# Performance work log

Measured on AMD Instinct MI355X. Metric: run time of the kernel, lower is better.

The kernel has to match this reference:

```python
import jax, jax.numpy as jnp
import numpy as np

B, L, D = 4, 512, 512
VOCAB = 32000
SEMB_NUM = 4
SEG = VOCAB // SEMB_NUM
TEMP = float(np.power(512, 0.5))  # sqrt(d_model)
NEG_INF = 1e9  # hparams.inf
INIT_RANGE = 0.1


def setup_inputs() -> dict:
    key = jax.random.key(0)
    k1, k2, k3 = jax.random.split(key, 3)
    q = jax.random.normal(k1, (B, L, D), dtype=jnp.float32)
    x_rank = jax.random.randint(k2, (B, L), 0, SEMB_NUM)
    emb = jax.random.uniform(k3, (VOCAB, D), dtype=jnp.float32,
                             minval=-INIT_RANGE, maxval=INIT_RANGE)
    return {"q": q, "x_rank": x_rank, "emb": emb}


def reference(q, x_rank, emb):
    # segment id of each vocab entry: [V]
    seg_id = jnp.arange(VOCAB) // SEG
    # mask == True means "blocked": token with x_rank==i only sees segment i
    mask = seg_id[None, None, :] != x_rank[:, :, None]          # [B, L, V]
    scores = jnp.einsum('bld,vd->blv', q, emb) / TEMP           # [B, L, V]
    scores = jnp.where(mask, -NEG_INF, scores)
    attn = jax.nn.softmax(scores, axis=-1)
    attn = jnp.where(mask, 0.0, attn)  # masked_fill_ after softmax (dropout=0, eval)
    ctx = jnp.einsum('blv,vd->bld', attn, emb)                  # [B, L, D]
    return ctx + q  # residual add (no char_gate)
```

## Files before the change

kernel.cpp:

```cpp
#include <hip/hip_runtime.h>
#include <math.h>


constexpr int Dm   = 512;
constexpr int SEG  = 8000;
constexpr int PSTR = 8064;
constexpr int NTOK = 2048;
constexpr int TIL  = 128;
constexpr int MAXTILES = 20;
constexpr int MAXSLOTS = MAXTILES * TIL;

constexpr size_t WS_META  = 8192;
constexpr size_t WS_PERM  = 8448;
constexpr size_t WS_IPERM = 20480;
constexpr size_t WS_QB8   = 32768;
constexpr size_t WS_EB8   = WS_QB8 + (size_t)MAXSLOTS * Dm;
constexpr size_t WS_OACC  = WS_EB8 + (size_t)32000 * Dm;
constexpr size_t WS_ET8   = WS_OACC + (size_t)8 * Dm * MAXSLOTS * 2;
constexpr size_t WS_P8    = WS_ET8 + (size_t)Dm * 32000;
constexpr size_t WS_DPART = WS_P8 + (size_t)MAXSLOTS * PSTR;

typedef __attribute__((ext_vector_type(4))) float f32x4;
typedef __attribute__((ext_vector_type(4))) unsigned int u32x4;
#define LDSP __attribute__((address_space(3)))
typedef LDSP unsigned char lds_u8;
typedef LDSP u32x4 lds_v4;
typedef LDSP int lds_i32;

static __device__ __forceinline__ ushort f2bf(float f) {
    union { float f; unsigned u; } v; v.f = f;
    unsigned r = v.u + 0x7FFF + ((v.u >> 16) & 1);
    return (ushort)(r >> 16);
}
static __device__ __forceinline__ float bf2f(ushort u) {
    union { unsigned u; float f; } v; v.u = ((unsigned)u) << 16;
    return v.f;
}
static __device__ __forceinline__ int pack_fp8x4(float a, float b, float c, float d) {
    int r = __builtin_amdgcn_cvt_pk_fp8_f32(a, b, 0, false);
    r = __builtin_amdgcn_cvt_pk_fp8_f32(c, d, r, true);
    return r;
}

#define WAIT0 asm volatile("s_waitcnt vmcnt(0)" ::: "memory")
#define LGKM0 asm volatile("s_waitcnt lgkmcnt(0)" ::: "memory")
#define BARX  { __builtin_amdgcn_s_barrier(); __builtin_amdgcn_sched_barrier(0); }

#define CSTEP(CA, CB)                                                          \
    _Pragma("unroll")                                                          \
    for (int ks = 0; ks < 4; ++ks) {                                           \
        const int cg = ks*2 + (quad >> 1), ho = (quad & 1) * 8;                \
        long A[4], B[4];                                                       \
        _Pragma("unroll")                                                      \
        for (int m = 0; m < 4; ++m) {                                          \
            const int row = rh*64 + m*16 + l15;                                \
            A[m] = *(const LDSP long*)((CA) + (row*8 + (cg ^ (row & 7)))*16 + ho); \
        }                                                                      \
        _Pragma("unroll")                                                      \
        for (int n = 0; n < 4; ++n) {                                          \
            const int row = th*64 + n*16 + l15;                                \
            B[n] = *(const LDSP long*)((CB) + (row*8 + (cg ^ (row & 7)))*16 + ho); \
        }                                                                      \
        __builtin_amdgcn_s_setprio(1);                                         \
        _Pragma("unroll")                                                      \
        for (int m = 0; m < 4; ++m)                                            \
            _Pragma("unroll")                                                  \
            for (int n = 0; n < 4; ++n)                                        \
                acc[m][n] = __builtin_amdgcn_mfma_f32_16x16x32_fp8_fp8(A[m], B[n], acc[m][n], 0, 0, 0); \
        __builtin_amdgcn_s_setprio(0);                                         \
    }

#define PSTEP(CA, CB, NA, NB, T)                                               \
    {                                                                          \
        u32x4 sv[8];                                                           \
        _Pragma("unroll")                                                      \
        for (int i = 0; i < 4; ++i) {                                          \
            sv[i]   = *(const u32x4*)(srcA[i] + (size_t)(T)*128);              \
            sv[4+i] = *(const u32x4*)(srcB[i] + (size_t)(T)*128);              \
        }                                                                      \
        CSTEP(CA, CB)                                                          \
        WAIT0;                                                                 \
        _Pragma("unroll")                                                      \
        for (int i = 0; i < 4; ++i) {                                          \
            *(lds_v4*)((NA) + dst[i]) = sv[i];                                 \
            *(lds_v4*)((NB) + dst[i]) = sv[4+i];                               \
        }                                                                      \
        LGKM0; BARX;                                                           \
    }

#define PROLOG(DA, DB)                                                         \
    {                                                                          \
        u32x4 sv[8];                                                           \
        _Pragma("unroll")                                                      \
        for (int i = 0; i < 4; ++i) {                                          \
            sv[i]   = *(const u32x4*)(srcA[i]);                                \
            sv[4+i] = *(const u32x4*)(srcB[i]);                                \
        }                                                                      \
        WAIT0;                                                                 \
        _Pragma("unroll")                                                      \
        for (int i = 0; i < 4; ++i) {                                          \
            *(lds_v4*)((DA) + dst[i]) = sv[i];                                 \
            *(lds_v4*)((DB) + dst[i]) = sv[4+i];                               \
        }                                                                      \
        LGKM0; BARX;                                                           \
    }

__global__ __launch_bounds__(256)
void k_conv(const float* __restrict__ emb, unsigned char* __restrict__ EB8,
            unsigned char* __restrict__ ET8,
            const int* __restrict__ xr, int* __restrict__ meta,
            int* __restrict__ perm, int* __restrict__ iperm) {
    __shared__ unsigned char sT[64 * 8 * 16];
    const int tid = threadIdx.x;
    if (blockIdx.x == 250) {
        if (blockIdx.y != 0) return;
        __shared__ int cnt[4], base[5], cur[4];
        if (tid < 4) { cnt[tid] = 0; cur[tid] = 0; }
        __syncthreads();
        for (int t = tid; t < NTOK; t += 256)
            atomicAdd(&cnt[xr[t]], 1);
        __syncthreads();
        if (tid == 0) {
            base[0] = 0;
            for (int r = 0; r < 4; ++r) base[r+1] = base[r] + ((cnt[r] + TIL - 1) / TIL) * TIL;
            for (int r = 0; r < 5; ++r) meta[r] = base[r];
        }
        __syncthreads();
        for (int s = tid; s < MAXSLOTS; s += 256) perm[s] = -1;
        __syncthreads();
        for (int t = tid; t < NTOK; t += 256) {
            int r = xr[t];
            int sl = base[r] + atomicAdd(&cur[r], 1);
            perm[sl] = t;
            iperm[t] = sl;
        }
        return;
    }
    const int r0 = blockIdx.x * 128, d0 = blockIdx.y * 64;
    {
        const int dq = tid & 15, ro = tid >> 4;
        int p[8];
        #pragma unroll
        for (int i = 0; i < 8; ++i) {
            float4 v = *(const float4*)(emb + (size_t)(r0 + ro*8 + i) * Dm + d0 + dq*4);
            p[i] = pack_fp8x4(v.x, v.y, v.z, v.w);
            *(int*)(EB8 + (size_t)(r0 + ro*8 + i) * Dm + d0 + dq*4) = p[i];
        }
        const int gr = ro >> 1, half = ro & 1;
        #pragma unroll
        for (int j = 0; j < 4; ++j) {
            const int d = dq*4 + j;
            unsigned long long t = 0;
            #pragma unroll
            for (int i = 0; i < 8; ++i)
                t |= ((unsigned long long)((p[i] >> (8*j)) & 0xff)) << (8*i);
            *(unsigned long long*)(sT + (d*8 + (gr ^ (d & 7))) * 16 + half * 8) = t;
        }
    }
    __syncthreads();
    {
        const int d = tid >> 2, rq = tid & 3;
        unsigned char* dst = ET8 + (size_t)(d0 + d) * 32000 + r0;
        #pragma unroll
        for (int b = 0; b < 2; ++b) {
            const int gr = rq * 2 + b;
            *(uint4*)(dst + gr * 16) = *(const uint4*)(sT + (d*8 + (gr ^ (d & 7))) * 16);
        }
    }
}

__global__ __launch_bounds__(256)
void k_qb(const float* __restrict__ q, const int* __restrict__ perm,
          unsigned char* __restrict__ Qb8) {
    const int slot = blockIdx.x * 8 + (threadIdx.x >> 5);
    const int ln = threadIdx.x & 31;
    const int tok = perm[slot];
    #pragma unroll
    for (int j = 0; j < 4; ++j) {
        const int c4 = ln + j * 32;
        int p = 0;
        if (tok >= 0) {
            float4 v = ((const float4*)q)[(size_t)tok * 128 + c4];
            p = pack_fp8x4(v.x, v.y, v.z, v.w);
        }
        ((int*)(Qb8 + (size_t)slot * Dm))[c4] = p;
    }
}

__global__ __launch_bounds__(256, 2)
void k_qk(const unsigned char* __restrict__ EB8, const unsigned char* __restrict__ Qb8,
          const int* __restrict__ meta, float* __restrict__ dpart,
          unsigned char* __restrict__ P8) {
    __shared__ unsigned char sA0[128 * 128];
    __shared__ unsigned char sB0[128 * 128];
    __shared__ unsigned char sA1[128 * 128];
    __shared__ unsigned char sB1[128 * 128];
    const int tid = threadIdx.x, lane = tid & 63, w = tid >> 6;
    const int g    = blockIdx.x & 7;
    const int rest = blockIdx.x >> 3;
    const int tt       = rest >> 3;
    const int rt_local = rest & 7;
    const int c = g * 8 + rt_local;
    const int slot0 = tt * TIL;
    const int b1 = meta[1], b2 = meta[2], b3 = meta[3], b4 = meta[4];
    if (slot0 >= b4) return;
    const int row0 = c * 128;
    if (row0 >= PSTR) return;
    const int rank = (slot0 >= b1) + (slot0 >= b2) + (slot0 >= b3);

    const unsigned char* srcA[4];
    const unsigned char* srcB[4];
    int dst[4];
    #pragma unroll
    for (int i = 0; i < 4; ++i) {
        const int gg = w * 256 + i * 64 + lane;
        const int r = gg >> 3, cg = gg & 7;
        int grow = row0 + r;
        if (grow >= SEG) grow = SEG - 1;
        srcA[i] = EB8 + (size_t)rank * SEG * Dm + (size_t)grow * Dm + cg * 16;
        srcB[i] = Qb8 + (size_t)(slot0 + r) * Dm + cg * 16;
        dst[i]  = (r * 8 + (cg ^ (r & 7))) * 16;
    }
    const int rh = w >> 1, th = w & 1, quad = lane >> 4, l15 = lane & 15;
    const float invT = 0.04419417382415922f;
    lds_u8* a0 = (lds_u8*)sA0; lds_u8* b0 = (lds_u8*)sB0;
    lds_u8* a1 = (lds_u8*)sA1; lds_u8* b1p = (lds_u8*)sB1;

    f32x4 acc[4][4] = {};
    PROLOG(a0, b0)
    PSTEP(a0, b0, a1, b1p, 1)
    PSTEP(a1, b1p, a0, b0, 2)
    PSTEP(a0, b0, a1, b1p, 3)
    CSTEP(a1, b1p)

    lds_i32* pT = (lds_i32*)sA0;
    float dsum[4] = {0.f, 0.f, 0.f, 0.f};
    #pragma unroll
    for (int m = 0; m < 4; ++m) {
        const int rloc = rh*64 + m*16 + quad*4;
        const int r4 = row0 + rloc;
        const int r4i = rloc >> 2;
        #pragma unroll
        for (int n = 0; n < 4; ++n) {
            const int slot_l = th*64 + n*16 + l15;
            int pv = 0;
            if (r4 < SEG) {
                float e0 = __expf(acc[m][n][0] * invT);
                float e1 = __expf(acc[m][n][1] * invT);
                float e2 = __expf(acc[m][n][2] * invT);
                float e3 = __expf(acc[m][n][3] * invT);
                pv = pack_fp8x4(e0, e1, e2, e3);
                dsum[n] += e0 + e1 + e2 + e3;
            }
            pT[slot_l * 32 + (r4i ^ ((slot_l & 7) << 2))] = pv;
        }
    }
    BARX;
    #pragma unroll
    for (int p = 0; p < 4; ++p) {
        const int sr = (tid >> 3) + p * 32;
        const int c4 = (tid & 7) * 4;
        const int i0 = sr * 32 + (c4 ^ ((sr & 7) << 2));
        u32x4 v = *(const LDSP u32x4*)(pT + i0);
        *(u32x4*)(P8 + (size_t)(slot0 + sr) * PSTR + row0 + (tid & 7) * 16) = v;
    }
    #pragma unroll
    for (int n = 0; n < 4; ++n) {
        float s = dsum[n];
        s += __shfl_xor(s, 16, 64);
        s += __shfl_xor(s, 32, 64);
        if (quad == 0)
            dpart[(size_t)(c * 2 + rh) * MAXSLOTS + slot0 + th*64 + n*16 + l15] = s;
    }
}

__global__ __launch_bounds__(256, 2)
void k_pv(const unsigned char* __restrict__ ET8, const unsigned char* __restrict__ P8,
          const int* __restrict__ meta, ushort* __restrict__ Oacc) {
    __shared__ unsigned char sA0[128 * 128];
    __shared__ unsigned char sB0[128 * 128];
    __shared__ unsigned char sA1[128 * 128];
    __shared__ unsigned char sB1[128 * 128];
    const int tid = threadIdx.x, lane = tid & 63, w = tid >> 6;
    const int z    = blockIdx.x & 7;
    const int rest = blockIdx.x >> 3;
    const int tt   = rest >> 2;
    const int dt   = rest & 3;
    const int slot0 = tt * TIL;
    const int b1 = meta[1], b2 = meta[2], b3 = meta[3], b4 = meta[4];
    if (slot0 >= b4) return;
    const int rank = (slot0 >= b1) + (slot0 >= b2) + (slot0 >= b3);
    const int d0 = dt * 128;
    const int kstart = z * 1024;
    const int nit = (z == 7) ? 7 : 8;

    const unsigned char* srcA[4];
    const unsigned char* srcB[4];
    int dst[4];
    #pragma unroll
    for (int i = 0; i < 4; ++i) {
        const int gg = w * 256 + i * 64 + lane;
        const int r = gg >> 3, cg = gg & 7;
        srcA[i] = ET8 + (size_t)(d0 + r) * 32000 + (size_t)rank * SEG + kstart + cg * 16;
        srcB[i] = P8 + (size_t)(slot0 + r) * PSTR + kstart + cg * 16;
        dst[i]  = (r * 8 + (cg ^ (r & 7))) * 16;
    }
    const int rh = w >> 1, th = w & 1, quad = lane >> 4, l15 = lane & 15;
    lds_u8* cA = (lds_u8*)sA0; lds_u8* cB = (lds_u8*)sB0;
    lds_u8* nA = (lds_u8*)sA1; lds_u8* nB = (lds_u8*)sB1;

    f32x4 acc[4][4] = {};
    PROLOG(cA, cB)
    for (int t = 1; t < nit; ++t) {
        PSTEP(cA, cB, nA, nB, t)
        lds_u8* tp;
        tp = cA; cA = nA; nA = tp;
        tp = cB; cB = nB; nB = tp;
    }
    CSTEP(cA, cB)

    ushort* Oz = Oacc + (size_t)z * MAXSLOTS * Dm;
    #pragma unroll
    for (int m = 0; m < 4; ++m) {
        const int d4 = d0 + rh*64 + m*16 + quad*4;
        #pragma unroll
        for (int n = 0; n < 4; ++n) {
            const int slot = slot0 + th*64 + n*16 + l15;
            unsigned long long u =
                  (unsigned long long)f2bf(acc[m][n][0])
                | ((unsigned long long)f2bf(acc[m][n][1]) << 16)
                | ((unsigned long long)f2bf(acc[m][n][2]) << 32)
                | ((unsigned long long)f2bf(acc[m][n][3]) << 48);
            *(unsigned long long*)(Oz + (size_t)slot * Dm + d4) = u;
        }
    }
}

__global__ __launch_bounds__(256)
void k_final(const float* __restrict__ q, const int* __restrict__ iperm,
             const float* __restrict__ dpart, const ushort* __restrict__ Oacc,
             float* __restrict__ out) {
    const int tk = threadIdx.x >> 5;
    const int dl = threadIdx.x & 31;
    const int token = blockIdx.x * 8 + tk;
    const int s = iperm[token];
    float ds = 0.f;
    #pragma unroll
    for (int r = 0; r < 4; ++r) {
        const int j = dl + r * 32;
        if (j < 126) ds += dpart[(size_t)j * MAXSLOTS + s];
    }
    ds += __shfl_xor(ds, 1, 64);
    ds += __shfl_xor(ds, 2, 64);
    ds += __shfl_xor(ds, 4, 64);
    ds += __shfl_xor(ds, 8, 64);
    ds += __shfl_xor(ds, 16, 64);
    const float inv = 1.0f / ds;
    const float* qrow = q + (size_t)token * Dm;
    float* orow = out + (size_t)token * Dm;
    #pragma unroll
    for (int p = 0; p < 4; ++p) {
        const int d = p * 128 + dl * 4;
        float a0 = 0.f, a1 = 0.f, a2 = 0.f, a3 = 0.f;
        #pragma unroll
        for (int z = 0; z < 8; ++z) {
            unsigned long long u = *(const unsigned long long*)
                (Oacc + ((size_t)z * MAXSLOTS + s) * Dm + d);
            a0 += bf2f((ushort)u);
            a1 += bf2f((ushort)(u >> 16));
            a2 += bf2f((ushort)(u >> 32));
            a3 += bf2f((ushort)(u >> 48));
        }
        float4 qv = *(const float4*)(qrow + d);
        float4 o;
        o.x = a0 * inv + qv.x; o.y = a1 * inv + qv.y;
        o.z = a2 * inv + qv.z; o.w = a3 * inv + qv.w;
        *(float4*)(orow + d) = o;
    }
}

extern "C" void kernel_launch(void* const* d_in, const int* in_sizes, int n_in,
                              void* d_out, int out_size, void* d_ws, size_t ws_size,
                              hipStream_t stream) {
    const float* q   = (const float*)d_in[0];
    const int*   xr  = (const int*)d_in[1];
    const float* emb = (const float*)d_in[2];
    float* out = (float*)d_out;
    char* ws = (char*)d_ws;

    int*    meta         = (int*)(ws + WS_META);
    int*    perm         = (int*)(ws + WS_PERM);
    int*    iperm        = (int*)(ws + WS_IPERM);
    unsigned char* Qb8   = (unsigned char*)(ws + WS_QB8);
    unsigned char* EB8   = (unsigned char*)(ws + WS_EB8);
    ushort* Oacc         = (ushort*)(ws + WS_OACC);
    unsigned char* ET8   = (unsigned char*)(ws + WS_ET8);
    unsigned char* P8    = (unsigned char*)(ws + WS_P8);
    float*  dpart        = (float*)(ws + WS_DPART);

    k_conv<<<dim3(251, 8), 256, 0, stream>>>(emb, EB8, ET8, xr, meta, perm, iperm);
    k_qb<<<MAXSLOTS / 8, 256, 0, stream>>>(q, perm, Qb8);
    k_qk<<<8 * 8 * MAXTILES, 256, 0, stream>>>(EB8, Qb8, meta, dpart, P8);
    k_pv<<<8 * 4 * MAXTILES, 256, 0, stream>>>(ET8, P8, meta, Oacc);
    k_final<<<NTOK / 8, 256, 0, stream>>>(q, iperm, dpart, Oacc, out);
}
```

Baseline: 166.6 us.

## Enlarge QK and PV GEMM tiles to 256 rows with 64-wide K steps

Both fp8 MFMA kernels move from 128x128 tiles with 128-byte K steps to 256x128 tiles with 64-byte K steps. Each warp now holds an 8x4 accumulator grid, and the LDS swizzle and staging layout are changed to match. The grid sizes are halved and the dpart partial count in the final reduction shrinks to match. The aim is more operand reuse per LDS load and fewer blocks. The cost is more accumulator registers, which may reduce occupancy, and fewer blocks to spread across the CUs.

```diff
diff --git a/kernel.cpp b/kernel.cpp
--- a/kernel.cpp
+++ b/kernel.cpp
@@ -46,62 +46,64 @@
 #define LGKM0 asm volatile("s_waitcnt lgkmcnt(0)" ::: "memory")
 #define BARX  { __builtin_amdgcn_s_barrier(); __builtin_amdgcn_sched_barrier(0); }
 
-#define CSTEP(CA, CB)                                                          \
+#define CSTEP8(CA, CB)                                                         \
     _Pragma("unroll")                                                          \
-    for (int ks = 0; ks < 4; ++ks) {                                           \
+    for (int ks = 0; ks < 2; ++ks) {                                           \
         const int cg = ks*2 + (quad >> 1), ho = (quad & 1) * 8;                \
-        long A[4], B[4];                                                       \
+        long A[8], B[4];                                                       \
         _Pragma("unroll")                                                      \
-        for (int m = 0; m < 4; ++m) {                                          \
-            const int row = rh*64 + m*16 + l15;                                \
-            A[m] = *(const LDSP long*)((CA) + (row*8 + (cg ^ (row & 7)))*16 + ho); \
+        for (int m = 0; m < 8; ++m) {                                          \
+            const int row = rh*128 + m*16 + l15;                               \
+            A[m] = *(const LDSP long*)((CA) + (row*4 + (cg ^ (row & 3)))*16 + ho); \
         }                                                                      \
         _Pragma("unroll")                                                      \
         for (int n = 0; n < 4; ++n) {                                          \
             const int row = th*64 + n*16 + l15;                                \
-            B[n] = *(const LDSP long*)((CB) + (row*8 + (cg ^ (row & 7)))*16 + ho); \
+            B[n] = *(const LDSP long*)((CB) + (row*4 + (cg ^ (row & 3)))*16 + ho); \
         }                                                                      \
         __builtin_amdgcn_s_setprio(1);                                         \
         _Pragma("unroll")                                                      \
-        for (int m = 0; m < 4; ++m)                                            \
+        for (int m = 0; m < 8; ++m)                                            \
             _Pragma("unroll")                                                  \
             for (int n = 0; n < 4; ++n)                                        \
                 acc[m][n] = __builtin_amdgcn_mfma_f32_16x16x32_fp8_fp8(A[m], B[n], acc[m][n], 0, 0, 0); \
         __builtin_amdgcn_s_setprio(0);                                         \
     }
 
-#define PSTEP(CA, CB, NA, NB, T)                                               \
+#define PSTEP8(CA, CB, NA, NB, T)                                              \
     {                                                                          \
-        u32x4 sv[8];                                                           \
-        _Pragma("unroll")                                                      \
-        for (int i = 0; i < 4; ++i) {                                          \
-            sv[i]   = *(const u32x4*)(srcA[i] + (size_t)(T)*128);              \
-            sv[4+i] = *(const u32x4*)(srcB[i] + (size_t)(T)*128);              \
-        }                                                                      \
-        CSTEP(CA, CB)                                                          \
+        u32x4 sa0 = *(const u32x4*)(srcA[0] + (size_t)(T)*64);                 \
+        u32x4 sa1 = *(const u32x4*)(srcA[1] + (size_t)(T)*64);                 \
+        u32x4 sa2 = *(const u32x4*)(srcA[2] + (size_t)(T)*64);                 \
+        u32x4 sa3 = *(const u32x4*)(srcA[3] + (size_t)(T)*64);                 \
+        u32x4 sb0 = *(const u32x4*)(srcB[0] + (size_t)(T)*64);                 \
+        u32x4 sb1 = *(const u32x4*)(srcB[1] + (size_t)(T)*64);                 \
+        CSTEP8(CA, CB)                                                         \
         WAIT0;                                                                 \
-        _Pragma("unroll")                                                      \
-        for (int i = 0; i < 4; ++i) {                                          \
-            *(lds_v4*)((NA) + dst[i]) = sv[i];                                 \
-            *(lds_v4*)((NB) + dst[i]) = sv[4+i];                               \
-        }                                                                      \
+        *(lds_v4*)((NA) + dstA[0]) = sa0;                                      \
+        *(lds_v4*)((NA) + dstA[1]) = sa1;                                      \
+        *(lds_v4*)((NA) + dstA[2]) = sa2;                                      \
+        *(lds_v4*)((NA) + dstA[3]) = sa3;                                      \
+        *(lds_v4*)((NB) + dstB[0]) = sb0;                                      \
+        *(lds_v4*)((NB) + dstB[1]) = sb1;                                      \
         LGKM0; BARX;                                                           \
     }
 
-#define PROLOG(DA, DB)                                                         \
+#define PROLOG8(DA, DB)                                                        \
     {                                                                          \
-        u32x4 sv[8];                                                           \
-        _Pragma("unroll")                                                      \
-        for (int i = 0; i < 4; ++i) {                                          \
-            sv[i]   = *(const u32x4*)(srcA[i]);                                \
-            sv[4+i] = *(const u32x4*)(srcB[i]);                                \
-        }                                                                      \
+        u32x4 sa0 = *(const u32x4*)(srcA[0]);                                  \
+        u32x4 sa1 = *(const u32x4*)(srcA[1]);                                  \
+        u32x4 sa2 = *(const u32x4*)(srcA[2]);                                  \
+        u32x4 sa3 = *(const u32x4*)(srcA[3]);                                  \
+        u32x4 sb0 = *(const u32x4*)(srcB[0]);                                  \
+        u32x4 sb1 = *(const u32x4*)(srcB[1]);                                  \
         WAIT0;                                                                 \
-        _Pragma("unroll")                                                      \
-        for (int i = 0; i < 4; ++i) {                                          \
-            *(lds_v4*)((DA) + dst[i]) = sv[i];                                 \
-            *(lds_v4*)((DB) + dst[i]) = sv[4+i];                               \
-        }                                                                      \
+        *(lds_v4*)((DA) + dstA[0]) = sa0;                                      \
+        *(lds_v4*)((DA) + dstA[1]) = sa1;                                      \
+        *(lds_v4*)((DA) + dstA[2]) = sa2;                                      \
+        *(lds_v4*)((DA) + dstA[3]) = sa3;                                      \
+        *(lds_v4*)((DB) + dstB[0]) = sb0;                                      \
+        *(lds_v4*)((DB) + dstB[1]) = sb1;                                      \
         LGKM0; BARX;                                                           \
     }
 
@@ -191,55 +193,63 @@
 void k_qk(const unsigned char* __restrict__ EB8, const unsigned char* __restrict__ Qb8,
           const int* __restrict__ meta, float* __restrict__ dpart,
           unsigned char* __restrict__ P8) {
-    __shared__ unsigned char sA0[128 * 128];
-    __shared__ unsigned char sB0[128 * 128];
-    __shared__ unsigned char sA1[128 * 128];
-    __shared__ unsigned char sB1[128 * 128];
+    __shared__ unsigned char smem[49152];
+    lds_u8* A0 = (lds_u8*)smem;
+    lds_u8* A1 = (lds_u8*)(smem + 16384);
+    lds_u8* B0 = (lds_u8*)(smem + 32768);
+    lds_u8* B1 = (lds_u8*)(smem + 40960);
     const int tid = threadIdx.x, lane = tid & 63, w = tid >> 6;
     const int g    = blockIdx.x & 7;
     const int rest = blockIdx.x >> 3;
-    const int tt       = rest >> 3;
-    const int rt_local = rest & 7;
-    const int c = g * 8 + rt_local;
+    const int tt   = rest >> 2;
+    const int rt   = rest & 3;
+    const int c = g * 4 + rt;
     const int slot0 = tt * TIL;
     const int b1 = meta[1], b2 = meta[2], b3 = meta[3], b4 = meta[4];
     if (slot0 >= b4) return;
-    const int row0 = c * 128;
-    if (row0 >= PSTR) return;
+    const int row0 = c * 256;
     const int rank = (slot0 >= b1) + (slot0 >= b2) + (slot0 >= b3);
 
-    const unsigned char* srcA[4];
-    const unsigned char* srcB[4];
-    int dst[4];
+    const unsigned char* srcA[4]; int dstA[4];
     #pragma unroll
     for (int i = 0; i < 4; ++i) {
-        const int gg = w * 256 + i * 64 + lane;
-        const int r = gg >> 3, cg = gg & 7;
+        const int gg = i * 256 + tid;
+        const int r = gg >> 2, cg = gg & 3;
         int grow = row0 + r;
         if (grow >= SEG) grow = SEG - 1;
         srcA[i] = EB8 + (size_t)rank * SEG * Dm + (size_t)grow * Dm + cg * 16;
+        dstA[i] = (r * 4 + (cg ^ (r & 3))) * 16;
+    }
+    const unsigned char* srcB[2]; int dstB[2];
+    #pragma unroll
+    for (int i = 0; i < 2; ++i) {
+        const int gg = i * 256 + tid;
+        const int r = gg >> 2, cg = gg & 3;
         srcB[i] = Qb8 + (size_t)(slot0 + r) * Dm + cg * 16;
-        dst[i]  = (r * 8 + (cg ^ (r & 7))) * 16;
+        dstB[i] = (r * 4 + (cg ^ (r & 3))) * 16;
     }
     const int rh = w >> 1, th = w & 1, quad = lane >> 4, l15 = lane & 15;
     const float invT = 0.04419417382415922f;
-    lds_u8* a0 = (lds_u8*)sA0; lds_u8* b0 = (lds_u8*)sB0;
-    lds_u8* a1 = (lds_u8*)sA1; lds_u8* b1p = (lds_u8*)sB1;
-
-    f32x4 acc[4][4] = {};
-    PROLOG(a0, b0)
-    PSTEP(a0, b0, a1, b1p, 1)
-    PSTEP(a1, b1p, a0, b0, 2)
-    PSTEP(a0, b0, a1, b1p, 3)
-    CSTEP(a1, b1p)
-
-    lds_i32* pT = (lds_i32*)sA0;
+
+    f32x4 acc[8][4] = {};
+    PROLOG8(A0, B0)
+    PSTEP8(A0, B0, A1, B1, 1)
+    PSTEP8(A1, B1, A0, B0, 2)
+    PSTEP8(A0, B0, A1, B1, 3)
+    PSTEP8(A1, B1, A0, B0, 4)
+    PSTEP8(A0, B0, A1, B1, 5)
+    PSTEP8(A1, B1, A0, B0, 6)
+    PSTEP8(A0, B0, A1, B1, 7)
+    CSTEP8(A1, B1)
+    BARX
+
+    lds_i32* pT = (lds_i32*)smem;
     float dsum[4] = {0.f, 0.f, 0.f, 0.f};
     #pragma unroll
-    for (int m = 0; m < 4; ++m) {
-        const int rloc = rh*64 + m*16 + quad*4;
+    for (int m = 0; m < 8; ++m) {
+        const int rloc = rh*128 + m*16 + quad*4;
         const int r4 = row0 + rloc;
-        const int r4i = rloc >> 2;
+        const int gi = (rloc >> 4);
         #pragma unroll
         for (int n = 0; n < 4; ++n) {
             const int slot_l = th*64 + n*16 + l15;
@@ -252,17 +262,19 @@
                 pv = pack_fp8x4(e0, e1, e2, e3);
                 dsum[n] += e0 + e1 + e2 + e3;
             }
-            pT[slot_l * 32 + (r4i ^ ((slot_l & 7) << 2))] = pv;
+            pT[slot_l * 64 + ((gi ^ (slot_l & 15)) << 2) + quad] = pv;
         }
     }
     BARX;
     #pragma unroll
-    for (int p = 0; p < 4; ++p) {
-        const int sr = (tid >> 3) + p * 32;
-        const int c4 = (tid & 7) * 4;
-        const int i0 = sr * 32 + (c4 ^ ((sr & 7) << 2));
-        u32x4 v = *(const LDSP u32x4*)(pT + i0);
-        *(u32x4*)(P8 + (size_t)(slot0 + sr) * PSTR + row0 + (tid & 7) * 16) = v;
+    for (int p = 0; p < 8; ++p) {
+        const int sr = (tid >> 4) + p * 16;
+        const int gi = tid & 15;
+        const int col = row0 + gi * 16;
+        if (col < PSTR) {
+            u32x4 v = *(const LDSP u32x4*)(pT + sr * 64 + ((gi ^ (sr & 15)) << 2));
+            *(u32x4*)(P8 + (size_t)(slot0 + sr) * PSTR + col) = v;
+        }
     }
     #pragma unroll
     for (int n = 0; n < 4; ++n) {
@@ -277,52 +289,56 @@
 __global__ __launch_bounds__(256, 2)
 void k_pv(const unsigned char* __restrict__ ET8, const unsigned char* __restrict__ P8,
           const int* __restrict__ meta, ushort* __restrict__ Oacc) {
-    __shared__ unsigned char sA0[128 * 128];
-    __shared__ unsigned char sB0[128 * 128];
-    __shared__ unsigned char sA1[128 * 128];
-    __shared__ unsigned char sB1[128 * 128];
+    __shared__ unsigned char smem[49152];
     const int tid = threadIdx.x, lane = tid & 63, w = tid >> 6;
     const int z    = blockIdx.x & 7;
     const int rest = blockIdx.x >> 3;
-    const int tt   = rest >> 2;
-    const int dt   = rest & 3;
+    const int tt   = rest >> 1;
+    const int dt   = rest & 1;
     const int slot0 = tt * TIL;
     const int b1 = meta[1], b2 = meta[2], b3 = meta[3], b4 = meta[4];
     if (slot0 >= b4) return;
     const int rank = (slot0 >= b1) + (slot0 >= b2) + (slot0 >= b3);
-    const int d0 = dt * 128;
+    const int d0 = dt * 256;
     const int kstart = z * 1024;
-    const int nit = (z == 7) ? 7 : 8;
-
-    const unsigned char* srcA[4];
-    const unsigned char* srcB[4];
-    int dst[4];
+    const int nit = (z == 7) ? 14 : 16;
+
+    const unsigned char* srcA[4]; int dstA[4];
     #pragma unroll
     for (int i = 0; i < 4; ++i) {
-        const int gg = w * 256 + i * 64 + lane;
-        const int r = gg >> 3, cg = gg & 7;
+        const int gg = i * 256 + tid;
+        const int r = gg >> 2, cg = gg & 3;
         srcA[i] = ET8 + (size_t)(d0 + r) * 32000 + (size_t)rank * SEG + kstart + cg * 16;
+        dstA[i] = (r * 4 + (cg ^ (r & 3))) * 16;
+    }
+    const unsigned char* srcB[2]; int dstB[2];
+    #pragma unroll
+    for (int i = 0; i < 2; ++i) {
+        const int gg = i * 256 + tid;
+        const int r = gg >> 2, cg = gg & 3;
         srcB[i] = P8 + (size_t)(slot0 + r) * PSTR + kstart + cg * 16;
-        dst[i]  = (r * 8 + (cg ^ (r & 7))) * 16;
+        dstB[i] = (r * 4 + (cg ^ (r & 3))) * 16;
     }
     const int rh = w >> 1, th = w & 1, quad = lane >> 4, l15 = lane & 15;
-    lds_u8* cA = (lds_u8*)sA0; lds_u8* cB = (lds_u8*)sB0;
-    lds_u8* nA = (lds_u8*)sA1; lds_u8* nB = (lds_u8*)sB1;
-
-    f32x4 acc[4][4] = {};
-    PROLOG(cA, cB)
+    lds_u8* cA = (lds_u8*)smem;
+    lds_u8* nA = (lds_u8*)(smem + 16384);
+    lds_u8* cB = (lds_u8*)(smem + 32768);
+    lds_u8* nB = (lds_u8*)(smem + 40960);
+
+    f32x4 acc[8][4] = {};
+    PROLOG8(cA, cB)
     for (int t = 1; t < nit; ++t) {
-        PSTEP(cA, cB, nA, nB, t)
+        PSTEP8(cA, cB, nA, nB, t)
         lds_u8* tp;
         tp = cA; cA = nA; nA = tp;
         tp = cB; cB = nB; nB = tp;
     }
-    CSTEP(cA, cB)
+    CSTEP8(cA, cB)
 
     ushort* Oz = Oacc + (size_t)z * MAXSLOTS * Dm;
     #pragma unroll
-    for (int m = 0; m < 4; ++m) {
-        const int d4 = d0 + rh*64 + m*16 + quad*4;
+    for (int m = 0; m < 8; ++m) {
+        const int d4 = d0 + rh*128 + m*16 + quad*4;
         #pragma unroll
         for (int n = 0; n < 4; ++n) {
             const int slot = slot0 + th*64 + n*16 + l15;
@@ -346,9 +362,9 @@
     const int s = iperm[token];
     float ds = 0.f;
     #pragma unroll
-    for (int r = 0; r < 4; ++r) {
+    for (int r = 0; r < 2; ++r) {
         const int j = dl + r * 32;
-        if (j < 126) ds += dpart[(size_t)j * MAXSLOTS + s];
+        ds += dpart[(size_t)j * MAXSLOTS + s];
     }
     ds += __shfl_xor(ds, 1, 64);
     ds += __shfl_xor(ds, 2, 64);
@@ -400,7 +416,7 @@
 
     k_conv<<<dim3(251, 8), 256, 0, stream>>>(emb, EB8, ET8, xr, meta, perm, iperm);
     k_qb<<<MAXSLOTS / 8, 256, 0, stream>>>(q, perm, Qb8);
-    k_qk<<<8 * 8 * MAXTILES, 256, 0, stream>>>(EB8, Qb8, meta, dpart, P8);
-    k_pv<<<8 * 4 * MAXTILES, 256, 0, stream>>>(ET8, P8, meta, Oacc);
+    k_qk<<<8 * 4 * MAXTILES, 256, 0, stream>>>(EB8, Qb8, meta, dpart, P8);
+    k_pv<<<8 * 2 * MAXTILES, 256, 0, stream>>>(ET8, P8, meta, Oacc);
     k_final<<<NTOK / 8, 256, 0, stream>>>(q, iperm, dpart, Oacc, out);
 }
```

Result: slower. 182.1 us (+9.3%).

## Pre-tile fp8 operands into MFMA fragment layout and load directly to registers

Applied to the files above, without the earlier changes.

The producer kernels (k_conv, k_qb, k_qk's P output) now write the fp8 embedding, transposed embedding, query and probability matrices in a blocked layout that matches the MFMA operand fragment order. The GEMM kernels k_qk and k_pv drop their LDS double buffering and load 16-byte fragments straight from global memory into registers, using a triple-buffered register pipeline with no barriers. This removes LDS staging, bank-conflict swizzles and block syncs in the hot loops. In exchange the loads depend on global latency and cache hits, register pressure rises, and the producers need an extra LDS transpose pass.

```diff
diff --git a/kernel.cpp b/kernel.cpp
--- a/kernel.cpp
+++ b/kernel.cpp
@@ -4,7 +4,6 @@
 
 constexpr int Dm   = 512;
 constexpr int SEG  = 8000;
-constexpr int PSTR = 8064;
 constexpr int NTOK = 2048;
 constexpr int TIL  = 128;
 constexpr int MAXTILES = 20;
@@ -14,17 +13,16 @@
 constexpr size_t WS_PERM  = 8448;
 constexpr size_t WS_IPERM = 20480;
 constexpr size_t WS_QB8   = 32768;
-constexpr size_t WS_EB8   = WS_QB8 + (size_t)MAXSLOTS * Dm;
-constexpr size_t WS_OACC  = WS_EB8 + (size_t)32000 * Dm;
-constexpr size_t WS_ET8   = WS_OACC + (size_t)8 * Dm * MAXSLOTS * 2;
-constexpr size_t WS_P8    = WS_ET8 + (size_t)Dm * 32000;
-constexpr size_t WS_DPART = WS_P8 + (size_t)MAXSLOTS * PSTR;
+constexpr size_t WS_EB8   = WS_QB8 + (size_t)160 * 8 * 1024;
+constexpr size_t WS_OACC  = WS_EB8 + (size_t)2000 * 8 * 1024;
+constexpr size_t WS_ET8   = WS_OACC + (size_t)8 * MAXSLOTS * Dm * 2;
+constexpr size_t WS_P8    = WS_ET8 + (size_t)32 * 504 * 1024;
+constexpr size_t WS_DPART = WS_P8 + (size_t)160 * 128 * 1024;
 
 typedef __attribute__((ext_vector_type(4))) float f32x4;
-typedef __attribute__((ext_vector_type(4))) unsigned int u32x4;
+typedef __attribute__((ext_vector_type(2))) long l64x2;
 #define LDSP __attribute__((address_space(3)))
 typedef LDSP unsigned char lds_u8;
-typedef LDSP u32x4 lds_v4;
 typedef LDSP int lds_i32;
 
 static __device__ __forceinline__ ushort f2bf(float f) {
@@ -42,75 +40,39 @@
     return r;
 }
 
-#define WAIT0 asm volatile("s_waitcnt vmcnt(0)" ::: "memory")
-#define LGKM0 asm volatile("s_waitcnt lgkmcnt(0)" ::: "memory")
-#define BARX  { __builtin_amdgcn_s_barrier(); __builtin_amdgcn_sched_barrier(0); }
-
-#define CSTEP(CA, CB)                                                          \
-    _Pragma("unroll")                                                          \
-    for (int ks = 0; ks < 4; ++ks) {                                           \
-        const int cg = ks*2 + (quad >> 1), ho = (quad & 1) * 8;                \
-        long A[4], B[4];                                                       \
+#define LOADT(BUF, T)                                                          \
+    { _Pragma("unroll")                                                        \
+      for (int i = 0; i < 4; ++i) {                                            \
+        BUF##a[i] = *(const l64x2*)(pA[i] + ((size_t)(T) << 10));              \
+        BUF##b[i] = *(const l64x2*)(pB[i] + ((size_t)(T) << 10));              \
+      }                                                                        \
+      __builtin_amdgcn_sched_barrier(0); }
+
+#define CONLY(BUF)                                                             \
+    { __builtin_amdgcn_s_setprio(1);                                           \
+      _Pragma("unroll")                                                        \
+      for (int m = 0; m < 4; ++m)                                              \
         _Pragma("unroll")                                                      \
-        for (int m = 0; m < 4; ++m) {                                          \
-            const int row = rh*64 + m*16 + l15;                                \
-            A[m] = *(const LDSP long*)((CA) + (row*8 + (cg ^ (row & 7)))*16 + ho); \
-        }                                                                      \
+        for (int n = 0; n < 4; ++n)                                            \
+            acc[m][n] = __builtin_amdgcn_mfma_f32_16x16x32_fp8_fp8(            \
+                BUF##a[m][0], BUF##b[n][0], acc[m][n], 0, 0, 0);               \
+      _Pragma("unroll")                                                        \
+      for (int m = 0; m < 4; ++m)                                              \
         _Pragma("unroll")                                                      \
-        for (int n = 0; n < 4; ++n) {                                          \
-            const int row = th*64 + n*16 + l15;                                \
-            B[n] = *(const LDSP long*)((CB) + (row*8 + (cg ^ (row & 7)))*16 + ho); \
-        }                                                                      \
-        __builtin_amdgcn_s_setprio(1);                                         \
-        _Pragma("unroll")                                                      \
-        for (int m = 0; m < 4; ++m)                                            \
-            _Pragma("unroll")                                                  \
-            for (int n = 0; n < 4; ++n)                                        \
-                acc[m][n] = __builtin_amdgcn_mfma_f32_16x16x32_fp8_fp8(A[m], B[n], acc[m][n], 0, 0, 0); \
-        __builtin_amdgcn_s_setprio(0);                                         \
-    }
-
-#define PSTEP(CA, CB, NA, NB, T)                                               \
-    {                                                                          \
-        u32x4 sv[8];                                                           \
-        _Pragma("unroll")                                                      \
-        for (int i = 0; i < 4; ++i) {                                          \
-            sv[i]   = *(const u32x4*)(srcA[i] + (size_t)(T)*128);              \
-            sv[4+i] = *(const u32x4*)(srcB[i] + (size_t)(T)*128);              \
-        }                                                                      \
-        CSTEP(CA, CB)                                                          \
-        WAIT0;                                                                 \
-        _Pragma("unroll")                                                      \
-        for (int i = 0; i < 4; ++i) {                                          \
-            *(lds_v4*)((NA) + dst[i]) = sv[i];                                 \
-            *(lds_v4*)((NB) + dst[i]) = sv[4+i];                               \
-        }                                                                      \
-        LGKM0; BARX;                                                           \
-    }
-
-#define PROLOG(DA, DB)                                                         \
-    {                                                                          \
-        u32x4 sv[8];                                                           \
-        _Pragma("unroll")                                                      \
-        for (int i = 0; i < 4; ++i) {                                          \
-            sv[i]   = *(const u32x4*)(srcA[i]);                                \
-            sv[4+i] = *(const u32x4*)(srcB[i]);                                \
-        }                                                                      \
-        WAIT0;                                                                 \
-        _Pragma("unroll")                                                      \
-        for (int i = 0; i < 4; ++i) {                                          \
-            *(lds_v4*)((DA) + dst[i]) = sv[i];                                 \
-            *(lds_v4*)((DB) + dst[i]) = sv[4+i];                               \
-        }                                                                      \
-        LGKM0; BARX;                                                           \
-    }
+        for (int n = 0; n < 4; ++n)                                            \
+            acc[m][n] = __builtin_amdgcn_mfma_f32_16x16x32_fp8_fp8(            \
+                BUF##a[m][1], BUF##b[n][1], acc[m][n], 0, 0, 0);               \
+      __builtin_amdgcn_s_setprio(0); }
+
+#define STEPQ(LB, T, CB)  LOADT(LB, T) CONLY(CB)
 
 __global__ __launch_bounds__(256)
-void k_conv(const float* __restrict__ emb, unsigned char* __restrict__ EB8,
-            unsigned char* __restrict__ ET8,
+void k_conv(const float* __restrict__ emb, unsigned char* __restrict__ EB8t,
+            unsigned char* __restrict__ ET8t,
             const int* __restrict__ xr, int* __restrict__ meta,
             int* __restrict__ perm, int* __restrict__ iperm) {
-    __shared__ unsigned char sT[64 * 8 * 16];
+    __shared__ unsigned char sE[8192];
+    __shared__ unsigned char sT8[8192];
     const int tid = threadIdx.x;
     if (blockIdx.x == 250) {
         if (blockIdx.y != 0) return;
@@ -136,7 +98,10 @@
         }
         return;
     }
-    const int r0 = blockIdx.x * 128, d0 = blockIdx.y * 64;
+    const int bx = blockIdx.x, by = blockIdx.y;
+    const int r0 = bx * 128, d0 = by * 64;
+    lds_u8* sEp = (lds_u8*)sE;
+    lds_u8* sTp = (lds_u8*)sT8;
     {
         const int dq = tid & 15, ro = tid >> 4;
         int p[8];
@@ -144,9 +109,10 @@
         for (int i = 0; i < 8; ++i) {
             float4 v = *(const float4*)(emb + (size_t)(r0 + ro*8 + i) * Dm + d0 + dq*4);
             p[i] = pack_fp8x4(v.x, v.y, v.z, v.w);
-            *(int*)(EB8 + (size_t)(r0 + ro*8 + i) * Dm + d0 + dq*4) = p[i];
-        }
-        const int gr = ro >> 1, half = ro & 1;
+            const int row = ro*8 + i;
+            const int s = ((row >> 3) ^ row) & 7;
+            *(lds_i32*)(sEp + row*64 + (((dq >> 1) ^ s) << 3) + (dq & 1)*4) = p[i];
+        }
         #pragma unroll
         for (int j = 0; j < 4; ++j) {
             const int d = dq*4 + j;
@@ -154,95 +120,125 @@
             #pragma unroll
             for (int i = 0; i < 8; ++i)
                 t |= ((unsigned long long)((p[i] >> (8*j)) & 0xff)) << (8*i);
-            *(unsigned long long*)(sT + (d*8 + (gr ^ (d & 7))) * 16 + half * 8) = t;
+            *(LDSP unsigned long long*)(sTp + d*128 + ((ro ^ (d & 15)) << 3)) = t;
         }
     }
     __syncthreads();
-    {
-        const int d = tid >> 2, rq = tid & 3;
-        unsigned char* dst = ET8 + (size_t)(d0 + d) * 32000 + r0;
-        #pragma unroll
-        for (int b = 0; b < 2; ++b) {
-            const int gr = rq * 2 + b;
-            *(uint4*)(dst + gr * 16) = *(const uint4*)(sT + (d*8 + (gr ^ (d & 7))) * 16);
-        }
+    #pragma unroll
+    for (int p = 0; p < 2; ++p) {
+        const int idx = p*256 + tid;
+        const int r16 = idx & 15, qq = (idx >> 4) & 3, rb = idx >> 6;
+        const int row = rb*16 + r16;
+        const int s = ((row >> 3) ^ row) & 7;
+        long lo = *(const LDSP long*)(sEp + row*64 + ((qq ^ s) << 3));
+        long hi = *(const LDSP long*)(sEp + row*64 + (((qq + 4) ^ s) << 3));
+        l64x2 v; v[0] = lo; v[1] = hi;
+        *(l64x2*)(EB8t + ((((size_t)(bx*8 + rb)) * 8 + by) << 10) + (qq*16 + r16)*16) = v;
+    }
+    #pragma unroll
+    for (int p = 0; p < 2; ++p) {
+        const int idx = p*256 + tid;
+        const int r16 = idx & 15, qq = (idx >> 4) & 3, tv = (idx >> 6) & 1, drb = idx >> 7;
+        const int d = drb*16 + r16;
+        long lo = *(const LDSP long*)(sTp + d*128 + (((tv*8 + qq) ^ (d & 15)) << 3));
+        long hi = *(const LDSP long*)(sTp + d*128 + (((tv*8 + 4 + qq) ^ (d & 15)) << 3));
+        l64x2 v; v[0] = lo; v[1] = hi;
+        *(l64x2*)(ET8t + (((size_t)(by*4 + drb) * 504 + bx*2 + tv) << 10) + (qq*16 + r16)*16) = v;
     }
 }
 
 __global__ __launch_bounds__(256)
 void k_qb(const float* __restrict__ q, const int* __restrict__ perm,
-          unsigned char* __restrict__ Qb8) {
-    const int slot = blockIdx.x * 8 + (threadIdx.x >> 5);
-    const int ln = threadIdx.x & 31;
-    const int tok = perm[slot];
-    #pragma unroll
-    for (int j = 0; j < 4; ++j) {
-        const int c4 = ln + j * 32;
-        int p = 0;
+          unsigned char* __restrict__ Qb8t) {
+    __shared__ unsigned char sQ[8192];
+    lds_u8* sQp = (lds_u8*)sQ;
+    const int tid = threadIdx.x;
+    const int srb = blockIdx.x;
+    const int r = tid >> 4, fidx = tid & 15;
+    const int tok = perm[srb*16 + r];
+    #pragma unroll
+    for (int j = 0; j < 8; ++j) {
+        const int f4 = fidx + j*16;
+        int pv = 0;
         if (tok >= 0) {
-            float4 v = ((const float4*)q)[(size_t)tok * 128 + c4];
-            p = pack_fp8x4(v.x, v.y, v.z, v.w);
-        }
-        ((int*)(Qb8 + (size_t)slot * Dm))[c4] = p;
+            float4 v = ((const float4*)q)[(size_t)tok * 128 + f4];
+            pv = pack_fp8x4(v.x, v.y, v.z, v.w);
+        }
+        *(lds_i32*)(sQp + r*512 + (((f4 >> 1) ^ (r & 7)) << 3) + (f4 & 1)*4) = pv;
+    }
+    __syncthreads();
+    #pragma unroll
+    for (int p = 0; p < 2; ++p) {
+        const int idx = p*256 + tid;
+        const int r16 = idx & 15, qq = (idx >> 4) & 3, td = idx >> 6;
+        long lo = *(const LDSP long*)(sQp + r16*512 + (((td*8 + qq) ^ (r16 & 7)) << 3));
+        long hi = *(const LDSP long*)(sQp + r16*512 + (((td*8 + 4 + qq) ^ (r16 & 7)) << 3));
+        l64x2 v; v[0] = lo; v[1] = hi;
+        *(l64x2*)(Qb8t + (((size_t)srb * 8 + td) << 10) + (qq*16 + r16)*16) = v;
     }
 }
 
 __global__ __launch_bounds__(256, 2)
-void k_qk(const unsigned char* __restrict__ EB8, const unsigned char* __restrict__ Qb8,
+void k_qk(const unsigned char* __restrict__ EB8t, const unsigned char* __restrict__ Qb8t,
           const int* __restrict__ meta, float* __restrict__ dpart,
-          unsigned char* __restrict__ P8) {
-    __shared__ unsigned char sA0[128 * 128];
-    __shared__ unsigned char sB0[128 * 128];
-    __shared__ unsigned char sA1[128 * 128];
-    __shared__ unsigned char sB1[128 * 128];
+          unsigned char* __restrict__ P8t) {
+    __shared__ unsigned char pT8[16384];
     const int tid = threadIdx.x, lane = tid & 63, w = tid >> 6;
     const int g    = blockIdx.x & 7;
     const int rest = blockIdx.x >> 3;
-    const int tt       = rest >> 3;
-    const int rt_local = rest & 7;
-    const int c = g * 8 + rt_local;
+    const int tt   = rest >> 3;
+    const int rt   = rest & 7;
+    const int c = g * 8 + rt;
     const int slot0 = tt * TIL;
     const int b1 = meta[1], b2 = meta[2], b3 = meta[3], b4 = meta[4];
     if (slot0 >= b4) return;
+    if (c == 63) {
+        #pragma unroll
+        for (int p = 0; p < 4; ++p) {
+            const int idx = p*256 + tid;
+            const int r16 = idx & 15, qq = (idx >> 4) & 3, tv = (idx >> 6) & 1, rb = idx >> 7;
+            l64x2 zz = {0, 0};
+            *(l64x2*)(P8t + ((((size_t)(slot0 >> 4) + rb) * 128 + 126 + tv) << 10)
+                          + (qq*16 + r16)*16) = zz;
+        }
+        return;
+    }
+    const int rank = (slot0 >= b1) + (slot0 >= b2) + (slot0 >= b3);
+    const int rh = w >> 1, th = w & 1, quad = lane >> 4, l15 = lane & 15;
     const int row0 = c * 128;
-    if (row0 >= PSTR) return;
-    const int rank = (slot0 >= b1) + (slot0 >= b2) + (slot0 >= b3);
-
-    const unsigned char* srcA[4];
-    const unsigned char* srcB[4];
-    int dst[4];
-    #pragma unroll
-    for (int i = 0; i < 4; ++i) {
-        const int gg = w * 256 + i * 64 + lane;
-        const int r = gg >> 3, cg = gg & 7;
-        int grow = row0 + r;
-        if (grow >= SEG) grow = SEG - 1;
-        srcA[i] = EB8 + (size_t)rank * SEG * Dm + (size_t)grow * Dm + cg * 16;
-        srcB[i] = Qb8 + (size_t)(slot0 + r) * Dm + cg * 16;
-        dst[i]  = (r * 8 + (cg ^ (r & 7))) * 16;
-    }
-    const int rh = w >> 1, th = w & 1, quad = lane >> 4, l15 = lane & 15;
+
+    const unsigned char* pA[4];
+    const unsigned char* pB[4];
+    #pragma unroll
+    for (int m = 0; m < 4; ++m) {
+        int rbl = c * 8 + rh * 4 + m;
+        if (rbl > 499) rbl = 499;
+        pA[m] = EB8t + (((size_t)(rank * 500 + rbl)) << 13) + lane * 16;
+        pB[m] = Qb8t + (((size_t)((slot0 >> 4) + th * 4 + m)) << 13) + lane * 16;
+    }
+    f32x4 acc[4][4] = {};
+    l64x2 b0a[4], b0b[4], b1a[4], b1b[4], b2a[4], b2b[4];
+    LOADT(b0, 0) LOADT(b1, 1)
+    STEPQ(b2, 2, b0)
+    STEPQ(b0, 3, b1)
+    STEPQ(b1, 4, b2)
+    STEPQ(b2, 5, b0)
+    STEPQ(b0, 6, b1)
+    STEPQ(b1, 7, b2)
+    CONLY(b0) CONLY(b1)
+
+    lds_u8* pTp = (lds_u8*)pT8;
     const float invT = 0.04419417382415922f;
-    lds_u8* a0 = (lds_u8*)sA0; lds_u8* b0 = (lds_u8*)sB0;
-    lds_u8* a1 = (lds_u8*)sA1; lds_u8* b1p = (lds_u8*)sB1;
-
-    f32x4 acc[4][4] = {};
-    PROLOG(a0, b0)
-    PSTEP(a0, b0, a1, b1p, 1)
-    PSTEP(a1, b1p, a0, b0, 2)
-    PSTEP(a0, b0, a1, b1p, 3)
-    CSTEP(a1, b1p)
-
-    lds_i32* pT = (lds_i32*)sA0;
     float dsum[4] = {0.f, 0.f, 0.f, 0.f};
     #pragma unroll
     for (int m = 0; m < 4; ++m) {
         const int rloc = rh*64 + m*16 + quad*4;
         const int r4 = row0 + rloc;
-        const int r4i = rloc >> 2;
+        const int gg = rloc >> 3;
+        const int hh = (quad & 1) * 4;
         #pragma unroll
         for (int n = 0; n < 4; ++n) {
-            const int slot_l = th*64 + n*16 + l15;
+            const int sl = th*64 + n*16 + l15;
             int pv = 0;
             if (r4 < SEG) {
                 float e0 = __expf(acc[m][n][0] * invT);
@@ -252,17 +248,21 @@
                 pv = pack_fp8x4(e0, e1, e2, e3);
                 dsum[n] += e0 + e1 + e2 + e3;
             }
-            pT[slot_l * 32 + (r4i ^ ((slot_l & 7) << 2))] = pv;
-        }
-    }
-    BARX;
+            *(lds_i32*)(pTp + sl*128 + ((gg ^ (sl & 15)) << 3) + hh) = pv;
+        }
+    }
+    __syncthreads();
     #pragma unroll
     for (int p = 0; p < 4; ++p) {
-        const int sr = (tid >> 3) + p * 32;
-        const int c4 = (tid & 7) * 4;
-        const int i0 = sr * 32 + (c4 ^ ((sr & 7) << 2));
-        u32x4 v = *(const LDSP u32x4*)(pT + i0);
-        *(u32x4*)(P8 + (size_t)(slot0 + sr) * PSTR + row0 + (tid & 7) * 16) = v;
+        const int idx = p*256 + tid;
+        const int r16 = idx & 15, qq = (idx >> 4) & 3, tv = (idx >> 6) & 1, rb = idx >> 7;
+        const int sl = rb*16 + r16;
+        const int g1 = tv*8 + qq;
+        long lo = *(const LDSP long*)(pTp + sl*128 + ((g1 ^ (sl & 15)) << 3));
+        long hi = *(const LDSP long*)(pTp + sl*128 + (((g1 + 4) ^ (sl & 15)) << 3));
+        l64x2 v; v[0] = lo; v[1] = hi;
+        *(l64x2*)(P8t + ((((size_t)(slot0 >> 4) + rb) * 128 + 2*c + tv) << 10)
+                      + (qq*16 + r16)*16) = v;
     }
     #pragma unroll
     for (int n = 0; n < 4; ++n) {
@@ -270,17 +270,13 @@
         s += __shfl_xor(s, 16, 64);
         s += __shfl_xor(s, 32, 64);
         if (quad == 0)
-            dpart[(size_t)(c * 2 + rh) * MAXSLOTS + slot0 + th*64 + n*16 + l15] = s;
+            dpart[(size_t)(c*2 + rh) * MAXSLOTS + slot0 + th*64 + n*16 + l15] = s;
     }
 }
 
 __global__ __launch_bounds__(256, 2)
-void k_pv(const unsigned char* __restrict__ ET8, const unsigned char* __restrict__ P8,
+void k_pv(const unsigned char* __restrict__ ET8t, const unsigned char* __restrict__ P8t,
           const int* __restrict__ meta, ushort* __restrict__ Oacc) {
-    __shared__ unsigned char sA0[128 * 128];
-    __shared__ unsigned char sB0[128 * 128];
-    __shared__ unsigned char sA1[128 * 128];
-    __shared__ unsigned char sB1[128 * 128];
     const int tid = threadIdx.x, lane = tid & 63, w = tid >> 6;
     const int z    = blockIdx.x & 7;
     const int rest = blockIdx.x >> 3;
@@ -291,33 +287,33 @@
     if (slot0 >= b4) return;
     const int rank = (slot0 >= b1) + (slot0 >= b2) + (slot0 >= b3);
     const int d0 = dt * 128;
-    const int kstart = z * 1024;
-    const int nit = (z == 7) ? 7 : 8;
-
-    const unsigned char* srcA[4];
-    const unsigned char* srcB[4];
-    int dst[4];
-    #pragma unroll
-    for (int i = 0; i < 4; ++i) {
-        const int gg = w * 256 + i * 64 + lane;
-        const int r = gg >> 3, cg = gg & 7;
-        srcA[i] = ET8 + (size_t)(d0 + r) * 32000 + (size_t)rank * SEG + kstart + cg * 16;
-        srcB[i] = P8 + (size_t)(slot0 + r) * PSTR + kstart + cg * 16;
-        dst[i]  = (r * 8 + (cg ^ (r & 7))) * 16;
-    }
     const int rh = w >> 1, th = w & 1, quad = lane >> 4, l15 = lane & 15;
-    lds_u8* cA = (lds_u8*)sA0; lds_u8* cB = (lds_u8*)sB0;
-    lds_u8* nA = (lds_u8*)sA1; lds_u8* nB = (lds_u8*)sB1;
-
+
+    const unsigned char* pA[4];
+    const unsigned char* pB[4];
+    #pragma unroll
+    for (int m = 0; m < 4; ++m) {
+        pA[m] = ET8t + ((((size_t)(dt*8 + rh*4 + m)) * 504 + rank*125 + z*16) << 10) + lane*16;
+        pB[m] = P8t + ((((size_t)((slot0 >> 4) + th*4 + m)) * 128 + z*16) << 10) + lane*16;
+    }
     f32x4 acc[4][4] = {};
-    PROLOG(cA, cB)
-    for (int t = 1; t < nit; ++t) {
-        PSTEP(cA, cB, nA, nB, t)
-        lds_u8* tp;
-        tp = cA; cA = nA; nA = tp;
-        tp = cB; cB = nB; nB = tp;
-    }
-    CSTEP(cA, cB)
+    l64x2 b0a[4], b0b[4], b1a[4], b1b[4], b2a[4], b2b[4];
+    LOADT(b0, 0) LOADT(b1, 1)
+    STEPQ(b2, 2, b0)
+    STEPQ(b0, 3, b1)
+    STEPQ(b1, 4, b2)
+    STEPQ(b2, 5, b0)
+    STEPQ(b0, 6, b1)
+    STEPQ(b1, 7, b2)
+    STEPQ(b2, 8, b0)
+    STEPQ(b0, 9, b1)
+    STEPQ(b1, 10, b2)
+    STEPQ(b2, 11, b0)
+    STEPQ(b0, 12, b1)
+    STEPQ(b1, 13, b2)
+    STEPQ(b2, 14, b0)
+    STEPQ(b0, 15, b1)
+    CONLY(b2) CONLY(b0)
 
     ushort* Oz = Oacc + (size_t)z * MAXSLOTS * Dm;
     #pragma unroll
@@ -391,16 +387,16 @@
     int*    meta         = (int*)(ws + WS_META);
     int*    perm         = (int*)(ws + WS_PERM);
     int*    iperm        = (int*)(ws + WS_IPERM);
-    unsigned char* Qb8   = (unsigned char*)(ws + WS_QB8);
-    unsigned char* EB8   = (unsigned char*)(ws + WS_EB8);
+    unsigned char* Qb8t  = (unsigned char*)(ws + WS_QB8);
+    unsigned char* EB8t  = (unsigned char*)(ws + WS_EB8);
     ushort* Oacc         = (ushort*)(ws + WS_OACC);
-    unsigned char* ET8   = (unsigned char*)(ws + WS_ET8);
-    unsigned char* P8    = (unsigned char*)(ws + WS_P8);
+    unsigned char* ET8t  = (unsigned char*)(ws + WS_ET8);
+    unsigned char* P8t   = (unsigned char*)(ws + WS_P8);
     float*  dpart        = (float*)(ws + WS_DPART);
 
-    k_conv<<<dim3(251, 8), 256, 0, stream>>>(emb, EB8, ET8, xr, meta, perm, iperm);
-    k_qb<<<MAXSLOTS / 8, 256, 0, stream>>>(q, perm, Qb8);
-    k_qk<<<8 * 8 * MAXTILES, 256, 0, stream>>>(EB8, Qb8, meta, dpart, P8);
-    k_pv<<<8 * 4 * MAXTILES, 256, 0, stream>>>(ET8, P8, meta, Oacc);
+    k_conv<<<dim3(251, 8), 256, 0, stream>>>(emb, EB8t, ET8t, xr, meta, perm, iperm);
+    k_qb<<<160, 256, 0, stream>>>(q, perm, Qb8t);
+    k_qk<<<8 * 8 * MAXTILES, 256, 0, stream>>>(EB8t, Qb8t, meta, dpart, P8t);
+    k_pv<<<8 * 4 * MAXTILES, 256, 0, stream>>>(ET8t, P8t, meta, Oacc);
     k_final<<<NTOK / 8, 256, 0, stream>>>(q, iperm, dpart, Oacc, out);
 }
```

Measured after the change: 155.3 us. -6.8%, faster.
